# Optimization experiments

Measured on AMD Instinct MI355X. Metric: run time of the kernel, lower is better.

Reference implementation:

```python
import jax, jax.numpy as jnp
import numpy as np

IN_FEATURES = 256
OUT_FEATURES = 64
ALPHA = 0.2  # leaky relu slope


def _xavier_uniform(key, shape, gain=1.414):
    fan_in, fan_out = shape[0], shape[1]
    limit = gain * np.sqrt(6.0 / (fan_in + fan_out))
    return jax.random.uniform(key, shape, jnp.float32, -limit, limit)


def setup_inputs() -> dict:
    key = jax.random.key(0)
    k_h, k_W, k_a = jax.random.split(key, 3)
    h = jax.random.normal(k_h, (8, 2048, IN_FEATURES), dtype=jnp.float32)
    W = _xavier_uniform(k_W, (IN_FEATURES, OUT_FEATURES))
    a = _xavier_uniform(k_a, (2 * OUT_FEATURES, 1))
    return {"h": h, "W": W, "a": a}


def reference(h, W, a):
    # h: [B, N, F_in], W: [F_in, D], a: [2D, 1]
    Wh = h @ W  # [B, N, D]
    D = Wh.shape[-1]
    a1 = a[:D, 0]   # attends to source node i (repeat_interleave side)
    a2 = a[D:, 0]   # attends to target node j (repeat side)
    f1 = Wh @ a1    # [B, N]
    f2 = Wh @ a2    # [B, N]
    # e[b, i, j] = leakyrelu(a1.Wh[b,i] + a2.Wh[b,j])  -- identical math to
    # the original's O(N^2 * 2D) repeat/concat, without materializing it.
    e = jax.nn.leaky_relu(f1[:, :, None] + f2[:, None, :], negative_slope=ALPHA)  # [B, N, N]
    # NOTE: original applies softmax over dim=1 (over i, per column j).
    attention = jax.nn.softmax(e, axis=1)  # [B, N, N]
    # dropout is identity in eval mode
    h_prime = jnp.einsum('bij,bjd->bid', attention, Wh)  # [B, N, D]
    return jax.nn.elu(h_prime)  # concat=True path
```

## Files before the change

### kernel.cpp

```cpp
#include <hip/hip_runtime.h>

#define B 8
#define N 2048
#define KF 256
#define DF 64
#define LOG2E 1.44269504088896340736f
#define IC 8
#define ICH (N / IC)

typedef __attribute__((ext_vector_type(8))) short short8;
typedef __attribute__((ext_vector_type(4))) float float4v;

__device__ __forceinline__ float fexp2(float x) {
#if __has_builtin(__builtin_amdgcn_exp2f)
    return __builtin_amdgcn_exp2f(x);
#else
    return exp2f(x);
#endif
}
__device__ __forceinline__ float flog2(float x) {
#if __has_builtin(__builtin_amdgcn_logf)
    return __builtin_amdgcn_logf(x);
#else
    return log2f(x);
#endif
}
__device__ __forceinline__ float eluf(float x) {
    return x > 0.f ? x : fexp2(x * LOG2E) - 1.0f;
}
__device__ __forceinline__ short bf16r(float x) {
    unsigned u = __float_as_uint(x);
    return (short)((u + 0x8000u) >> 16);
}
#define DOT4(c, u, p) \
    p = fmaf(c.x, u.x, fmaf(c.y, u.y, fmaf(c.z, u.z, fmaf(c.w, u.w, p))));

__global__ __launch_bounds__(256) void k_wh(const float* __restrict__ h,
                                            const float* __restrict__ W,
                                            const float* __restrict__ a,
                                            short* __restrict__ WhT,
                                            float* __restrict__ f1,
                                            float* __restrict__ f2) {
    __shared__ __align__(16) unsigned char smem[34816];
    short* lwt  = (short*)smem;
    float* lv   = (float*)(smem + 32768);
    float* lred = (float*)smem;
    float* lp   = (float*)(smem + 16896);

    int t = threadIdx.x;
    int wv = t >> 6, lane = t & 63;
    int n15 = lane & 15, q = lane >> 4;
    int bx = blockIdx.x;

    const float* hr = h + ((long)bx * 64 + n15) * KF + wv * 64 + q * 8;
    float4 c0 = *(const float4*)(hr);
    float4 c1 = *(const float4*)(hr + 4);
    float4 c2 = *(const float4*)(hr + 32);
    float4 c3 = *(const float4*)(hr + 36);

    {
        const float4* wr4 = (const float4*)(W + t * DF);
        float s1 = 0.f, s2 = 0.f;
        #pragma unroll
        for (int c = 0; c < 16; c++) {
            float4 w4 = wr4[c];
            float4 a1v = *(const float4*)(a + 4 * c);
            float4 a2v = *(const float4*)(a + DF + 4 * c);
            lwt[(4 * c + 0) * 256 + t] = bf16r(w4.x);
            lwt[(4 * c + 1) * 256 + t] = bf16r(w4.y);
            lwt[(4 * c + 2) * 256 + t] = bf16r(w4.z);
            lwt[(4 * c + 3) * 256 + t] = bf16r(w4.w);
            s1 = fmaf(w4.x, a1v.x, fmaf(w4.y, a1v.y, fmaf(w4.z, a1v.z, fmaf(w4.w, a1v.w, s1))));
            s2 = fmaf(w4.x, a2v.x, fmaf(w4.y, a2v.y, fmaf(w4.z, a2v.z, fmaf(w4.w, a2v.w, s2))));
        }
        lv[t] = s1;
        lv[256 + t] = s2;
    }
    __syncthreads();

    const short* bq = lwt + n15 * 256 + wv * 64 + q * 8;
    short8 s0b0 = *(const short8*)(bq);
    short8 s0b1 = *(const short8*)(bq + 16 * 256);
    short8 s0b2 = *(const short8*)(bq + 32 * 256);
    short8 s0b3 = *(const short8*)(bq + 48 * 256);
    short8 s1b0 = *(const short8*)(bq + 32);
    short8 s1b1 = *(const short8*)(bq + 16 * 256 + 32);
    short8 s1b2 = *(const short8*)(bq + 32 * 256 + 32);
    short8 s1b3 = *(const short8*)(bq + 48 * 256 + 32);
    const float* vv = lv + wv * 64 + q * 8;
    float4 u00 = *(const float4*)(vv);
    float4 u01 = *(const float4*)(vv + 4);
    float4 u10 = *(const float4*)(vv + 32);
    float4 u11 = *(const float4*)(vv + 36);
    float4 x00 = *(const float4*)(vv + 256);
    float4 x01 = *(const float4*)(vv + 256 + 4);
    float4 x10 = *(const float4*)(vv + 256 + 32);
    float4 x11 = *(const float4*)(vv + 256 + 36);
    __syncthreads();

    #pragma unroll
    for (int rt = 0; rt < 4; rt++) {
        float4 m0, m1, m2, m3;
        if (rt < 3) {
            const float* hn = hr + (rt + 1) * 16 * KF;
            m0 = *(const float4*)(hn);
            m1 = *(const float4*)(hn + 4);
            m2 = *(const float4*)(hn + 32);
            m3 = *(const float4*)(hn + 36);
        }
        float p1 = 0.f, p2 = 0.f;
        DOT4(c0, u00, p1) DOT4(c1, u01, p1) DOT4(c2, u10, p1) DOT4(c3, u11, p1)
        DOT4(c0, x00, p2) DOT4(c1, x01, p2) DOT4(c2, x10, p2) DOT4(c3, x11, p2)

        short8 af0 = { bf16r(c0.x), bf16r(c0.y), bf16r(c0.z), bf16r(c0.w),
                       bf16r(c1.x), bf16r(c1.y), bf16r(c1.z), bf16r(c1.w) };
        short8 af1 = { bf16r(c2.x), bf16r(c2.y), bf16r(c2.z), bf16r(c2.w),
                       bf16r(c3.x), bf16r(c3.y), bf16r(c3.z), bf16r(c3.w) };
        float4v acc0 = {0.f, 0.f, 0.f, 0.f}, acc1 = acc0, acc2 = acc0, acc3 = acc0;
        acc0 = __builtin_amdgcn_mfma_f32_16x16x32_bf16(af0, s0b0, acc0, 0, 0, 0);
        acc0 = __builtin_amdgcn_mfma_f32_16x16x32_bf16(af1, s1b0, acc0, 0, 0, 0);
        acc1 = __builtin_amdgcn_mfma_f32_16x16x32_bf16(af0, s0b1, acc1, 0, 0, 0);
        acc1 = __builtin_amdgcn_mfma_f32_16x16x32_bf16(af1, s1b1, acc1, 0, 0, 0);
        acc2 = __builtin_amdgcn_mfma_f32_16x16x32_bf16(af0, s0b2, acc2, 0, 0, 0);
        acc2 = __builtin_amdgcn_mfma_f32_16x16x32_bf16(af1, s1b2, acc2, 0, 0, 0);
        acc3 = __builtin_amdgcn_mfma_f32_16x16x32_bf16(af0, s0b3, acc3, 0, 0, 0);
        acc3 = __builtin_amdgcn_mfma_f32_16x16x32_bf16(af1, s1b3, acc3, 0, 0, 0);

        #define STASH(nb, A)                                                  \
            {                                                                 \
                _Pragma("unroll")                                             \
                for (int r = 0; r < 4; r++)                                   \
                    lred[wv * 1056 + (q * 4 + r) * 66 + nb * 16 + n15] = A[r]; \
            }
        STASH(0, acc0) STASH(1, acc1) STASH(2, acc2) STASH(3, acc3)
        #undef STASH
        p1 += __shfl_xor(p1, 16, 64); p1 += __shfl_xor(p1, 32, 64);
        p2 += __shfl_xor(p2, 16, 64); p2 += __shfl_xor(p2, 32, 64);
        if (q == 0) { lp[wv * 16 + n15] = p1; lp[64 + wv * 16 + n15] = p2; }
        __syncthreads();

        long i0 = (long)bx * 64 + rt * 16;
        int d = t & 63, ig = t >> 6;
        int bb = (int)(i0 >> 11);
        int il = (int)(i0 & (N - 1));
        float s0 = 0.f, s1 = 0.f, s2 = 0.f, s3 = 0.f;
        #pragma unroll
        for (int w = 0; w < 4; w++) {
            const float* lr = lred + w * 1056 + (ig * 4) * 66 + d;
            s0 += lr[0]; s1 += lr[66]; s2 += lr[132]; s3 += lr[198];
        }
        short4 pk = make_short4(bf16r(s0), bf16r(s1), bf16r(s2), bf16r(s3));
        int jj = il + ig * 4;
        *(short4*)(WhT + (((long)bb * 8 + (jj >> 8)) * 64 + d) * 256 + (jj & 255)) = pk;

        if (t < 16) {
            f1[i0 + t] = lp[t] + lp[16 + t] + lp[32 + t] + lp[48 + t];
        } else if (t < 32) {
            int tt = t + 48;
            f2[i0 + t - 16] = lp[tt] + lp[16 + tt] + lp[32 + tt] + lp[48 + tt];
        }
        __syncthreads();
        c0 = m0; c1 = m1; c2 = m2; c3 = m3;
    }
}

__global__ __launch_bounds__(256) void k_denom(const float* __restrict__ f1,
                                               const float* __restrict__ f2,
                                               float* __restrict__ dpart) {
    __shared__ float lf1[ICH];
    int t = threadIdx.x;
    int b = blockIdx.z, ic = blockIdx.y;
    int j = blockIdx.x * 256 + t;
    lf1[t] = f1[b * N + ic * ICH + t];
    __syncthreads();
    float f2j = f2[b * N + j];
    float s = 0.f;
    for (int ii = 0; ii < ICH; ii++) {
        float e = (lf1[ii] + f2j) * LOG2E;
        s += fexp2(fmaxf(e, 0.2f * e));
    }
    dpart[((long)ic * B + b) * N + j] = s;
}

__global__ __launch_bounds__(256) void k_attn(const short* __restrict__ WhT,
                                              const float* __restrict__ f1,
                                              const float* __restrict__ f2,
                                              const float* __restrict__ dpart,
                                              float* __restrict__ out) {
    __shared__ uint4 ls[64][33];
    __shared__ float2 lc[2][256];
    int t = threadIdx.x;
    int wv = t >> 6, lane = t & 63;
    int n15 = lane & 15, q = lane >> 4;
    int it = blockIdx.x, b = blockIdx.y;
    int i0 = it * 64 + wv * 16;

    float f1L = f1[b * N + i0 + n15] * LOG2E;
    const uint4* wsrc = (const uint4*)WhT + (long)b * 8 * 2048;
    const float* f2b = f2 + b * N;
    const float* dpb = dpart + b * N;

    uint4 r0, r1, r2, r3, r4, r5, r6, r7;
    float pf2, pd0, pd1, pd2, pd3, pd4, pd5, pd6, pd7;

    #define LOADC(cc) {                                     \
        const uint4* gp = wsrc + (cc) * 2048;               \
        r0 = gp[t];        r1 = gp[256 + t];                \
        r2 = gp[512 + t];  r3 = gp[768 + t];                \
        r4 = gp[1024 + t]; r5 = gp[1280 + t];               \
        r6 = gp[1536 + t]; r7 = gp[1792 + t];               \
    }
    #define LOADP(cc) {                                     \
        int jb2 = (cc) * 256 + t;                           \
        pf2 = f2b[jb2];                                     \
        pd0 = dpb[jb2];              pd1 = dpb[16384 + jb2];\
        pd2 = dpb[2 * 16384 + jb2];  pd3 = dpb[3 * 16384 + jb2]; \
        pd4 = dpb[4 * 16384 + jb2];  pd5 = dpb[5 * 16384 + jb2]; \
        pd6 = dpb[6 * 16384 + jb2];  pd7 = dpb[7 * 16384 + jb2]; \
    }
    #define STOREC() {                                      \
        int rb = t >> 5, cl = t & 31;                       \
        ls[rb][cl] = r0;      ls[8 + rb][cl] = r1;          \
        ls[16 + rb][cl] = r2; ls[24 + rb][cl] = r3;         \
        ls[32 + rb][cl] = r4; ls[40 + rb][cl] = r5;         \
        ls[48 + rb][cl] = r6; ls[56 + rb][cl] = r7;         \
    }
    #define LCC(buf) {                                      \
        float den = ((pd0 + pd1) + (pd2 + pd3)) + ((pd4 + pd5) + (pd6 + pd7)); \
        lc[buf][t] = make_float2(pf2 * LOG2E, -flog2(den)); \
    }

    LOADC(0) LOADP(0)
    STOREC() LCC(0)
    __syncthreads();

    float4v acc0 = {0.f, 0.f, 0.f, 0.f}, acc1 = acc0, acc2 = acc0, acc3 = acc0;

    for (int c = 0; c < 8; c++) {
        int cur = c & 1;
        if (c < 7) { LOADC(c + 1) LOADP(c + 1) }

        const short* lsS = (const short*)&ls[0][0];
        const float4* lcf = (const float4*)&lc[cur][0];
        #pragma unroll
        for (int js = 0; js < 8; js++) {
            const float4* cp4 = lcf + js * 16 + q * 4;
            float4 p01 = cp4[0], p23 = cp4[1], p45 = cp4[2], p67 = cp4[3];
            short8 af;
            #define PENT(F2L, LS2, DI)                        \
                {                                             \
                    float t0 = f1L + (F2L);                   \
                    float l2 = fmaxf(t0, 0.2f * t0);          \
                    af[DI] = bf16r(fexp2(l2 + (LS2)));        \
                }
            PENT(p01.x, p01.y, 0) PENT(p01.z, p01.w, 1)
            PENT(p23.x, p23.y, 2) PENT(p23.z, p23.w, 3)
            PENT(p45.x, p45.y, 4) PENT(p45.z, p45.w, 5)
            PENT(p67.x, p67.y, 6) PENT(p67.z, p67.w, 7)
            #undef PENT

            const short* bp = lsS + js * 32 + q * 8;
            short8 b0 = *(const short8*)(bp + (n15 +  0) * 264);
            short8 b1 = *(const short8*)(bp + (n15 + 16) * 264);
            short8 b2 = *(const short8*)(bp + (n15 + 32) * 264);
            short8 b3 = *(const short8*)(bp + (n15 + 48) * 264);

            acc0 = __builtin_amdgcn_mfma_f32_16x16x32_bf16(af, b0, acc0, 0, 0, 0);
            acc1 = __builtin_amdgcn_mfma_f32_16x16x32_bf16(af, b1, acc1, 0, 0, 0);
            acc2 = __builtin_amdgcn_mfma_f32_16x16x32_bf16(af, b2, acc2, 0, 0, 0);
            acc3 = __builtin_amdgcn_mfma_f32_16x16x32_bf16(af, b3, acc3, 0, 0, 0);
        }

        if (c < 7) {
            __syncthreads();
            STOREC() LCC((c + 1) & 1)
            __syncthreads();
        }
    }
    #undef LOADC
    #undef LOADP
    #undef STOREC
    #undef LCC

    float* ob = out + ((long)b * N + i0 + q * 4) * DF + n15;
    #pragma unroll
    for (int r = 0; r < 4; r++) {
        ob[r * DF + 0]  = eluf(acc0[r]);
        ob[r * DF + 16] = eluf(acc1[r]);
        ob[r * DF + 32] = eluf(acc2[r]);
        ob[r * DF + 48] = eluf(acc3[r]);
    }
}

extern "C" void kernel_launch(void* const* d_in, const int* in_sizes, int n_in,
                              void* d_out, int out_size, void* d_ws, size_t ws_size,
                              hipStream_t stream) {
    const float* h = (const float*)d_in[0];
    const float* W = (const float*)d_in[1];
    const float* a = (const float*)d_in[2];
    float* out = (float*)d_out;

    char* ws = (char*)d_ws;
    const size_t NB = (size_t)B * N;
    size_t off = 0;
    short* WhT   = (short*)(ws + off); off += NB * DF * sizeof(short);
    float* f1    = (float*)(ws + off); off += NB * sizeof(float);
    float* f2    = (float*)(ws + off); off += NB * sizeof(float);
    float* dpart = (float*)(ws + off); off += (size_t)IC * NB * sizeof(float);
    (void)off; (void)ws_size;

    k_wh<<<NB / 64, 256, 0, stream>>>(h, W, a, WhT, f1, f2);
    k_denom<<<dim3(N / 256, IC, B), 256, 0, stream>>>(f1, f2, dpart);
    k_attn<<<dim3(N / 64, B), 256, 0, stream>>>(WhT, f1, f2, dpart, out);
}
```

Baseline: 102.2 us.

## Split attention j-range across two wave groups, halve Wh tile rows, vectorize denom

The attention kernel now runs 512 threads per block, with two groups of four waves. Each group handles half of the j range, and the partial accumulators are reduced through shared memory in a new epilogue that also writes the output with coalesced float4 stores. The WhT layout is changed to 128-column chunks to match. The Wh projection kernel processes 32 rows per block instead of 64, doubling the grid, and the denominator loop folds LOG2E into an fma and reads f1 as float4. The aim is to raise occupancy and parallelism, at the cost of an extra LDS reduction and more blocks.

```diff
diff --git a/kernel.cpp b/kernel.cpp
--- a/kernel.cpp
+++ b/kernel.cpp
@@ -52,7 +52,7 @@
     int n15 = lane & 15, q = lane >> 4;
     int bx = blockIdx.x;
 
-    const float* hr = h + ((long)bx * 64 + n15) * KF + wv * 64 + q * 8;
+    const float* hr = h + ((long)bx * 32 + n15) * KF + wv * 64 + q * 8;
     float4 c0 = *(const float4*)(hr);
     float4 c1 = *(const float4*)(hr + 4);
     float4 c2 = *(const float4*)(hr + 32);
@@ -99,10 +99,10 @@
     __syncthreads();
 
     #pragma unroll
-    for (int rt = 0; rt < 4; rt++) {
+    for (int rt = 0; rt < 2; rt++) {
         float4 m0, m1, m2, m3;
-        if (rt < 3) {
-            const float* hn = hr + (rt + 1) * 16 * KF;
+        if (rt < 1) {
+            const float* hn = hr + 16 * KF;
             m0 = *(const float4*)(hn);
             m1 = *(const float4*)(hn + 4);
             m2 = *(const float4*)(hn + 32);
@@ -139,7 +139,7 @@
         if (q == 0) { lp[wv * 16 + n15] = p1; lp[64 + wv * 16 + n15] = p2; }
         __syncthreads();
 
-        long i0 = (long)bx * 64 + rt * 16;
+        long i0 = (long)bx * 32 + rt * 16;
         int d = t & 63, ig = t >> 6;
         int bb = (int)(i0 >> 11);
         int il = (int)(i0 & (N - 1));
@@ -151,7 +151,7 @@
         }
         short4 pk = make_short4(bf16r(s0), bf16r(s1), bf16r(s2), bf16r(s3));
         int jj = il + ig * 4;
-        *(short4*)(WhT + (((long)bb * 8 + (jj >> 8)) * 64 + d) * 256 + (jj & 255)) = pk;
+        *(short4*)(WhT + (((long)bb * 16 + (jj >> 7)) * 64 + d) * 128 + (jj & 127)) = pk;
 
         if (t < 16) {
             f1[i0 + t] = lp[t] + lp[16 + t] + lp[32 + t] + lp[48 + t];
@@ -173,61 +173,72 @@
     int j = blockIdx.x * 256 + t;
     lf1[t] = f1[b * N + ic * ICH + t];
     __syncthreads();
-    float f2j = f2[b * N + j];
+    float f2j = f2[b * N + j] * LOG2E;
     float s = 0.f;
-    for (int ii = 0; ii < ICH; ii++) {
-        float e = (lf1[ii] + f2j) * LOG2E;
-        s += fexp2(fmaxf(e, 0.2f * e));
+    const float4* lf4 = (const float4*)lf1;
+    for (int ii = 0; ii < ICH / 4; ii++) {
+        float4 v = lf4[ii];
+        float e0 = fmaf(v.x, LOG2E, f2j);
+        float e1 = fmaf(v.y, LOG2E, f2j);
+        float e2 = fmaf(v.z, LOG2E, f2j);
+        float e3 = fmaf(v.w, LOG2E, f2j);
+        s += fexp2(fmaxf(e0, 0.2f * e0));
+        s += fexp2(fmaxf(e1, 0.2f * e1));
+        s += fexp2(fmaxf(e2, 0.2f * e2));
+        s += fexp2(fmaxf(e3, 0.2f * e3));
     }
     dpart[((long)ic * B + b) * N + j] = s;
 }
 
-__global__ __launch_bounds__(256) void k_attn(const short* __restrict__ WhT,
+__global__ __launch_bounds__(512) void k_attn(const short* __restrict__ WhT,
                                               const float* __restrict__ f1,
                                               const float* __restrict__ f2,
                                               const float* __restrict__ dpart,
                                               float* __restrict__ out) {
-    __shared__ uint4 ls[64][33];
-    __shared__ float2 lc[2][256];
+    __shared__ uint4 ls[2][64 * 17];
+    __shared__ float2 lc[2][2][128];
     int t = threadIdx.x;
     int wv = t >> 6, lane = t & 63;
+    int g = wv >> 2, wg = wv & 3, lt = t & 255;
     int n15 = lane & 15, q = lane >> 4;
     int it = blockIdx.x, b = blockIdx.y;
-    int i0 = it * 64 + wv * 16;
+    int i0 = it * 64 + wg * 16;
 
     float f1L = f1[b * N + i0 + n15] * LOG2E;
-    const uint4* wsrc = (const uint4*)WhT + (long)b * 8 * 2048;
-    const float* f2b = f2 + b * N;
-    const float* dpb = dpart + b * N;
-
-    uint4 r0, r1, r2, r3, r4, r5, r6, r7;
+    const uint4* wsrc = (const uint4*)WhT + ((long)b * 16 + g * 8) * 1024;
+    const float* f2b = f2 + b * N + g * 1024;
+    const float* dpb = dpart + b * N + g * 1024;
+
+    uint4 r0, r1, r2, r3;
     float pf2, pd0, pd1, pd2, pd3, pd4, pd5, pd6, pd7;
 
     #define LOADC(cc) {                                     \
-        const uint4* gp = wsrc + (cc) * 2048;               \
-        r0 = gp[t];        r1 = gp[256 + t];                \
-        r2 = gp[512 + t];  r3 = gp[768 + t];                \
-        r4 = gp[1024 + t]; r5 = gp[1280 + t];               \
-        r6 = gp[1536 + t]; r7 = gp[1792 + t];               \
+        const uint4* gp = wsrc + (cc) * 1024;               \
+        r0 = gp[lt];       r1 = gp[256 + lt];               \
+        r2 = gp[512 + lt]; r3 = gp[768 + lt];               \
     }
     #define LOADP(cc) {                                     \
-        int jb2 = (cc) * 256 + t;                           \
-        pf2 = f2b[jb2];                                     \
-        pd0 = dpb[jb2];              pd1 = dpb[16384 + jb2];\
-        pd2 = dpb[2 * 16384 + jb2];  pd3 = dpb[3 * 16384 + jb2]; \
-        pd4 = dpb[4 * 16384 + jb2];  pd5 = dpb[5 * 16384 + jb2]; \
-        pd6 = dpb[6 * 16384 + jb2];  pd7 = dpb[7 * 16384 + jb2]; \
+        if (lt < 128) {                                     \
+            int jb2 = (cc) * 128 + lt;                      \
+            pf2 = f2b[jb2];                                 \
+            pd0 = dpb[jb2];              pd1 = dpb[16384 + jb2]; \
+            pd2 = dpb[2 * 16384 + jb2];  pd3 = dpb[3 * 16384 + jb2]; \
+            pd4 = dpb[4 * 16384 + jb2];  pd5 = dpb[5 * 16384 + jb2]; \
+            pd6 = dpb[6 * 16384 + jb2];  pd7 = dpb[7 * 16384 + jb2]; \
+        }                                                   \
     }
     #define STOREC() {                                      \
-        int rb = t >> 5, cl = t & 31;                       \
-        ls[rb][cl] = r0;      ls[8 + rb][cl] = r1;          \
-        ls[16 + rb][cl] = r2; ls[24 + rb][cl] = r3;         \
-        ls[32 + rb][cl] = r4; ls[40 + rb][cl] = r5;         \
-        ls[48 + rb][cl] = r6; ls[56 + rb][cl] = r7;         \
+        int rb = lt >> 4, cl = lt & 15;                     \
+        ls[g][rb * 17 + cl] = r0;                           \
+        ls[g][(16 + rb) * 17 + cl] = r1;                    \
+        ls[g][(32 + rb) * 17 + cl] = r2;                    \
+        ls[g][(48 + rb) * 17 + cl] = r3;                    \
     }
     #define LCC(buf) {                                      \
-        float den = ((pd0 + pd1) + (pd2 + pd3)) + ((pd4 + pd5) + (pd6 + pd7)); \
-        lc[buf][t] = make_float2(pf2 * LOG2E, -flog2(den)); \
+        if (lt < 128) {                                     \
+            float den = ((pd0 + pd1) + (pd2 + pd3)) + ((pd4 + pd5) + (pd6 + pd7)); \
+            lc[g][buf][lt] = make_float2(pf2 * LOG2E, -flog2(den)); \
+        }                                                   \
     }
 
     LOADC(0) LOADP(0)
@@ -240,10 +251,10 @@
         int cur = c & 1;
         if (c < 7) { LOADC(c + 1) LOADP(c + 1) }
 
-        const short* lsS = (const short*)&ls[0][0];
-        const float4* lcf = (const float4*)&lc[cur][0];
+        const short* lsS = (const short*)&ls[g][0];
+        const float4* lcf = (const float4*)&lc[g][cur][0];
         #pragma unroll
-        for (int js = 0; js < 8; js++) {
+        for (int js = 0; js < 4; js++) {
             const float4* cp4 = lcf + js * 16 + q * 4;
             float4 p01 = cp4[0], p23 = cp4[1], p45 = cp4[2], p67 = cp4[3];
             short8 af;
@@ -260,10 +271,10 @@
             #undef PENT
 
             const short* bp = lsS + js * 32 + q * 8;
-            short8 b0 = *(const short8*)(bp + (n15 +  0) * 264);
-            short8 b1 = *(const short8*)(bp + (n15 + 16) * 264);
-            short8 b2 = *(const short8*)(bp + (n15 + 32) * 264);
-            short8 b3 = *(const short8*)(bp + (n15 + 48) * 264);
+            short8 b0 = *(const short8*)(bp + (n15 +  0) * 136);
+            short8 b1 = *(const short8*)(bp + (n15 + 16) * 136);
+            short8 b2 = *(const short8*)(bp + (n15 + 32) * 136);
+            short8 b3 = *(const short8*)(bp + (n15 + 48) * 136);
 
             acc0 = __builtin_amdgcn_mfma_f32_16x16x32_bf16(af, b0, acc0, 0, 0, 0);
             acc1 = __builtin_amdgcn_mfma_f32_16x16x32_bf16(af, b1, acc1, 0, 0, 0);
@@ -282,14 +293,33 @@
     #undef STOREC
     #undef LCC
 
-    float* ob = out + ((long)b * N + i0 + q * 4) * DF + n15;
-    #pragma unroll
-    for (int r = 0; r < 4; r++) {
-        ob[r * DF + 0]  = eluf(acc0[r]);
-        ob[r * DF + 16] = eluf(acc1[r]);
-        ob[r * DF + 32] = eluf(acc2[r]);
-        ob[r * DF + 48] = eluf(acc3[r]);
-    }
+    __syncthreads();
+    float* epi = (float*)&ls[0][0];
+    #define ESTASH(nb, A)                                                    \
+        {                                                                    \
+            _Pragma("unroll")                                                \
+            for (int r = 0; r < 4; r++)                                      \
+                epi[g * 4224 + (wg * 16 + q * 4 + r) * 66 + nb * 16 + n15] = A[r]; \
+        }
+    ESTASH(0, acc0) ESTASH(1, acc1) ESTASH(2, acc2) ESTASH(3, acc3)
+    #undef ESTASH
+    __syncthreads();
+
+    int row = t >> 3, d0 = (t & 7) * 8;
+    const float* e0p = epi + row * 66 + d0;
+    const float* e1p = epi + 4224 + row * 66 + d0;
+    float4 a0 = *(const float4*)(e0p);
+    float4 a1 = *(const float4*)(e0p + 4);
+    float4 b0 = *(const float4*)(e1p);
+    float4 b1 = *(const float4*)(e1p + 4);
+    float4 o0, o1;
+    o0.x = eluf(a0.x + b0.x); o0.y = eluf(a0.y + b0.y);
+    o0.z = eluf(a0.z + b0.z); o0.w = eluf(a0.w + b0.w);
+    o1.x = eluf(a1.x + b1.x); o1.y = eluf(a1.y + b1.y);
+    o1.z = eluf(a1.z + b1.z); o1.w = eluf(a1.w + b1.w);
+    float* op = out + ((long)b * N + it * 64 + row) * DF + d0;
+    *(float4*)(op) = o0;
+    *(float4*)(op + 4) = o1;
 }
 
 extern "C" void kernel_launch(void* const* d_in, const int* in_sizes, int n_in,
@@ -309,7 +339,7 @@
     float* dpart = (float*)(ws + off); off += (size_t)IC * NB * sizeof(float);
     (void)off; (void)ws_size;
 
-    k_wh<<<NB / 64, 256, 0, stream>>>(h, W, a, WhT, f1, f2);
+    k_wh<<<NB / 32, 256, 0, stream>>>(h, W, a, WhT, f1, f2);
     k_denom<<<dim3(N / 256, IC, B), 256, 0, stream>>>(f1, f2, dpart);
-    k_attn<<<dim3(N / 64, B), 256, 0, stream>>>(WhT, f1, f2, dpart, out);
-}
+    k_attn<<<dim3(N / 64, B), 512, 0, stream>>>(WhT, f1, f2, dpart, out);
+}
```

New measurement: 97.82 us. 4.2% less time.
